# Optimization experiments

Hardware: AMD Instinct MI355X
Metric: run time of the kernel (lower is better)

The kernel has to match this reference:

```python
import jax, jax.numpy as jnp
import numpy as np
import math

DX = DZ = DATTN = DOUT = 1024
LX = LZ = 4096

def setup_inputs() -> dict:
    key = jax.random.key(0)
    ks = jax.random.split(key, 6)
    X = jax.random.normal(ks[0], (DX, LX), dtype=jnp.float32)
    Z = jax.random.normal(ks[1], (DZ, LZ), dtype=jnp.float32)
    mask = jax.random.randint(ks[2], (LZ, LX), 0, 2) > 0  # bool (lz, lx)
    Wq = jax.random.normal(ks[3], (DATTN, DX), dtype=jnp.float32) / math.sqrt(DATTN)
    bq = jnp.zeros((DATTN, 1), dtype=jnp.float32)
    Wk = jax.random.normal(ks[4], (DATTN, DZ), dtype=jnp.float32) / math.sqrt(DATTN)
    bk = jnp.zeros((DATTN, 1), dtype=jnp.float32)
    Wv = jax.random.normal(ks[5], (DOUT, DZ), dtype=jnp.float32) / math.sqrt(DOUT)
    bv = jnp.zeros((DOUT, 1), dtype=jnp.float32)
    return {"X": X, "Z": Z, "mask": mask, "Wq": Wq, "bq": bq,
            "Wk": Wk, "bk": bk, "Wv": Wv, "bv": bv}

def reference(X, Z, mask, Wq, bq, Wk, bk, Wv, bv):
    dattn_sqrt = math.sqrt(Wq.shape[0])
    q = Wq @ X + bq                      # (dattn, lx)
    k = Wk @ Z + bk                      # (dattn, lz)
    v = Wv @ Z + bv                      # (dout, lz)
    score = k.T @ q                      # (lz, lx)
    # masked_fill with -1000 happens BEFORE scaling, matching the original
    score = jnp.where(mask, score, jnp.float32(-1000.0))
    attn = jax.nn.softmax(score / dattn_sqrt, axis=0)  # softmax over lz (dim 0)
    return v @ attn                      # (dout, lx)
```

## Files before the change

kernel.cpp:

```cpp
#include <hip/hip_runtime.h>
#include <hip/hip_bf16.h>
#include <math.h>

constexpr int DXc = 1024;
constexpr int DZc = 1024;
constexpr int LXc = 4096;
constexpr int LZc = 4096;
constexpr int DAc = 1024;
constexpr int DOc = 1024;

typedef __attribute__((ext_vector_type(8))) short bf16x8;
typedef __attribute__((ext_vector_type(4))) float f32x4;

__device__ __forceinline__ ushort f2bf(float f) {
    __hip_bfloat16 h = __float2bfloat16(f);
    return *reinterpret_cast<ushort*>(&h);
}
__device__ __forceinline__ float bf2f(ushort u) {
    return __builtin_bit_cast(float, (unsigned)u << 16);
}

enum BiasMode { BIAS_NONE, BIAS_M, BIAS_N };

__device__ __forceinline__ void gemm_core(
    const ushort* __restrict__ A, const ushort* __restrict__ B,
    int K, int lda, int ldb, int m0, int n0, int kbase,
    ushort* As, ushort* Bs, f32x4 (*acc)[4])
{
    constexpr int BK = 32;
    const int tid = threadIdx.x;
    const int wv  = tid >> 6;
    const int wm  = (wv >> 1) * 64;
    const int wn  = (wv & 1) * 64;
    const int ln  = tid & 63;
    const int lrow = ln & 15;
    const int quad = ln >> 4;

    const int srow = tid >> 2;
    const int sseg = (tid & 3) * 8;
    const ushort* Ag = A + (size_t)(m0 + srow) * lda + sseg + kbase;
    const ushort* Bg = B + (size_t)(n0 + srow) * ldb + sseg + kbase;
    ushort* AsW = As + wv * 512;
    ushort* BsW = Bs + wv * 512;

    for (int k0 = 0; k0 < K; k0 += BK) {
        __syncthreads();
        __builtin_amdgcn_global_load_lds(
            (const __attribute__((address_space(1))) void*)(Ag + k0),
            (__attribute__((address_space(3))) void*)(AsW), 16, 0, 0);
        __builtin_amdgcn_global_load_lds(
            (const __attribute__((address_space(1))) void*)(Ag + (size_t)64 * lda + k0),
            (__attribute__((address_space(3))) void*)(AsW + 2048), 16, 0, 0);
        __builtin_amdgcn_global_load_lds(
            (const __attribute__((address_space(1))) void*)(Bg + k0),
            (__attribute__((address_space(3))) void*)(BsW), 16, 0, 0);
        __builtin_amdgcn_global_load_lds(
            (const __attribute__((address_space(1))) void*)(Bg + (size_t)64 * ldb + k0),
            (__attribute__((address_space(3))) void*)(BsW + 2048), 16, 0, 0);
        __syncthreads();

        bf16x8 af[4], bfr[4];
        #pragma unroll
        for (int t = 0; t < 4; ++t) {
            af[t]  = *reinterpret_cast<const bf16x8*>(&As[(wm + t * 16 + lrow) * BK + quad * 8]);
            bfr[t] = *reinterpret_cast<const bf16x8*>(&Bs[(wn + t * 16 + lrow) * BK + quad * 8]);
        }
        #pragma unroll
        for (int mi = 0; mi < 4; ++mi)
            #pragma unroll
            for (int nj = 0; nj < 4; ++nj)
                acc[mi][nj] = __builtin_amdgcn_mfma_f32_16x16x32_bf16(
                    af[mi], bfr[nj], acc[mi][nj], 0, 0, 0);
    }
}

template<BiasMode BMODE>
__device__ __forceinline__ void epi_bias_bf16(
    f32x4 (*acc)[4], const float* __restrict__ bias,
    ushort* __restrict__ C, int ldc, int m0, int n0)
{
    const int tid = threadIdx.x;
    const int wv  = tid >> 6;
    const int wm  = (wv >> 1) * 64;
    const int wn  = (wv & 1) * 64;
    const int lrow = tid & 15;
    const int quad = (tid & 63) >> 4;
    #pragma unroll
    for (int mi = 0; mi < 4; ++mi)
        #pragma unroll
        for (int r = 0; r < 4; ++r) {
            const int m = m0 + wm + mi * 16 + quad * 4 + r;
            const float bm = (BMODE == BIAS_M) ? bias[m] : 0.0f;
            #pragma unroll
            for (int nj = 0; nj < 4; ++nj) {
                const int n = n0 + wn + nj * 16 + lrow;
                const float v = acc[mi][nj][r] + ((BMODE == BIAS_N) ? bias[n] : bm);
                C[(size_t)m * ldc + n] = f2bf(v);
            }
        }
}

__global__ __launch_bounds__(256)
void proj_kernel(const ushort* __restrict__ XT, const ushort* __restrict__ ZT,
                 const ushort* __restrict__ Wqb, const ushort* __restrict__ Wkb,
                 const ushort* __restrict__ Wvb,
                 const float* __restrict__ bq, const float* __restrict__ bk,
                 const float* __restrict__ bv,
                 ushort* __restrict__ qT, ushort* __restrict__ kT,
                 ushort* __restrict__ vB)
{
    __shared__ __align__(16) ushort As[128 * 32];
    __shared__ __align__(16) ushort Bs[128 * 32];
    f32x4 acc[4][4] = {};
    int b = blockIdx.x;
    if (b < 256) {
        const int m0 = (b >> 3) * 128, n0 = (b & 7) * 128;
        gemm_core(XT, Wqb, DXc, DXc, DXc, m0, n0, 0, As, Bs, acc);
        epi_bias_bf16<BIAS_N>(acc, bq, qT, DAc, m0, n0);
    } else if (b < 512) {
        b -= 256;
        const int m0 = (b >> 3) * 128, n0 = (b & 7) * 128;
        gemm_core(ZT, Wkb, DZc, DZc, DZc, m0, n0, 0, As, Bs, acc);
        epi_bias_bf16<BIAS_N>(acc, bk, kT, DAc, m0, n0);
    } else {
        b -= 512;
        const int m0 = (b >> 5) * 128, n0 = (b & 31) * 128;
        gemm_core(Wvb, ZT, DZc, DZc, DZc, m0, n0, 0, As, Bs, acc);
        epi_bias_bf16<BIAS_M>(acc, bv, vB, LZc, m0, n0);
    }
}

__global__ __launch_bounds__(256)
void score_kernel(const ushort* __restrict__ qT, const ushort* __restrict__ kT,
                  ushort* __restrict__ sTb, const unsigned* __restrict__ bits,
                  float* __restrict__ rowsum)
{
    __shared__ __align__(16) ushort As[128 * 32];
    __shared__ __align__(16) ushort Bs[128 * 32];
    f32x4 acc[4][4] = {};
    const int b = blockIdx.x;
    const int m0 = (b >> 5) * 128, n0 = (b & 31) * 128;
    gemm_core(qT, kT, DAc, DAc, DAc, m0, n0, 0, As, Bs, acc);

    const int tid = threadIdx.x;
    const int wv  = tid >> 6;
    const int wm  = (wv >> 1) * 64;
    const int wn  = (wv & 1) * 64;
    const int lrow = tid & 15;
    const int quad = (tid & 63) >> 4;
    constexpr float scale = 1.0f / 32.0f;
    const int wbase = (n0 + wn) >> 5;

    #pragma unroll
    for (int mi = 0; mi < 4; ++mi) {
        #pragma unroll
        for (int r = 0; r < 4; ++r) {
            const int m = m0 + wm + mi * 16 + quad * 4 + r;
            const unsigned w0 = bits[(size_t)m * 128 + wbase];
            const unsigned w1 = bits[(size_t)m * 128 + wbase + 1];
            float rsum = 0.0f;
            #pragma unroll
            for (int nj = 0; nj < 4; ++nj) {
                const int nn = nj * 16 + lrow;
                const unsigned wsel = (nn < 32) ? w0 : w1;
                const bool mk = (wsel >> (nn & 31)) & 1u;
                float p = mk ? __expf(acc[mi][nj][r] * scale - 10.0f) : 0.0f;
                const ushort pb = f2bf(p);
                sTb[(size_t)m * LZc + (n0 + wn + nn)] = pb;
                rsum += bf2f(pb);
            }
            #pragma unroll
            for (int d = 1; d < 16; d <<= 1)
                rsum += __shfl_xor(rsum, d, 64);
            if (lrow == 0) atomicAdd(&rowsum[m], rsum);
        }
    }
}

__global__ __launch_bounds__(256)
void out_kernel(const ushort* __restrict__ vB, const ushort* __restrict__ sTb,
                float* __restrict__ P)
{
    __shared__ __align__(16) ushort As[128 * 32];
    __shared__ __align__(16) ushort Bs[128 * 32];
    f32x4 acc[4][4] = {};
    const int m0 = blockIdx.y * 128, n0 = blockIdx.x * 128;
    gemm_core(vB, sTb, LZc / 4, LZc, LZc, m0, n0, blockIdx.z * (LZc / 4), As, Bs, acc);

    float* Cf = P + (size_t)blockIdx.z * DOc * LXc;
    const int tid = threadIdx.x;
    const int wv  = tid >> 6;
    const int wm  = (wv >> 1) * 64;
    const int wn  = (wv & 1) * 64;
    const int lrow = tid & 15;
    const int quad = (tid & 63) >> 4;
    #pragma unroll
    for (int mi = 0; mi < 4; ++mi)
        #pragma unroll
        for (int r = 0; r < 4; ++r) {
            const int m = m0 + wm + mi * 16 + quad * 4 + r;
            #pragma unroll
            for (int nj = 0; nj < 4; ++nj)
                Cf[(size_t)m * LXc + (n0 + wn + nj * 16 + lrow)] = acc[mi][nj][r];
        }
}

__global__ __launch_bounds__(256)
void prep_kernel(const float* __restrict__ X, const float* __restrict__ Z,
                 const float* __restrict__ Wq, const float* __restrict__ Wk,
                 const float* __restrict__ Wv, const int* __restrict__ mask,
                 ushort* __restrict__ XT, ushort* __restrict__ ZT,
                 ushort* __restrict__ Wqb, ushort* __restrict__ Wkb,
                 ushort* __restrict__ Wvb, unsigned* __restrict__ bits)
{
    __shared__ float tile[32][33];
    const int tid = threadIdx.x;
    int b = blockIdx.x;

    if (b < 8192) {
        const float* in  = (b < 4096) ? X : Z;
        ushort*      out = (b < 4096) ? XT : ZT;
        const int local = b & 4095;
        const int c0 = (local & 127) * 32, r0 = (local >> 7) * 32;
        const int tx = tid & 31, ty = tid >> 5;
        #pragma unroll
        for (int i = 0; i < 32; i += 8)
            tile[ty + i][tx] = in[(size_t)(r0 + ty + i) * LXc + c0 + tx];
        __syncthreads();
        #pragma unroll
        for (int i = 0; i < 32; i += 8)
            out[(size_t)(c0 + ty + i) * DXc + r0 + tx] = f2bf(tile[tx][ty + i]);
        return;
    }
    if (b < 11264) {
        b -= 8192;
        const float* in  = (b < 1024) ? Wq : (b < 2048) ? Wk : Wv;
        ushort*      out = (b < 1024) ? Wqb : (b < 2048) ? Wkb : Wvb;
        const size_t i = ((size_t)(b & 1023) * 256 + tid) * 4;
        float4 f = *reinterpret_cast<const float4*>(in + i);
        ushort4 u;
        u.x = f2bf(f.x); u.y = f2bf(f.y); u.z = f2bf(f.z); u.w = f2bf(f.w);
        *reinterpret_cast<ushort4*>(out + i) = u;
        return;
    }
    b -= 11264;
    const int xb = b & 15, zb = b >> 4;
    const int x  = xb * 256 + tid;
    const int z0 = zb * 32;
    unsigned w = 0;
    #pragma unroll 8
    for (int i = 0; i < 32; ++i)
        w |= (mask[(size_t)(z0 + i) * LXc + x] != 0 ? 1u : 0u) << i;
    bits[(size_t)x * (LZc / 32) + zb] = w;
}

__global__ __launch_bounds__(256)
void reduce_kernel(const float* __restrict__ P, const float* __restrict__ rowsum,
                   float* __restrict__ out)
{
    constexpr size_t total = (size_t)DOc * LXc;
    const size_t i = ((size_t)blockIdx.x * 256 + threadIdx.x) * 4;
    float4 s = *reinterpret_cast<const float4*>(P + i);
    #pragma unroll
    for (int p = 1; p < 4; ++p) {
        const float4 t = *reinterpret_cast<const float4*>(P + (size_t)p * total + i);
        s.x += t.x; s.y += t.y; s.z += t.z; s.w += t.w;
    }
    const float4 l = *reinterpret_cast<const float4*>(rowsum + (i & (LXc - 1)));
    s.x /= fmaxf(l.x, 1e-30f);
    s.y /= fmaxf(l.y, 1e-30f);
    s.z /= fmaxf(l.z, 1e-30f);
    s.w /= fmaxf(l.w, 1e-30f);
    *reinterpret_cast<float4*>(out + i) = s;
}

extern "C" void kernel_launch(void* const* d_in, const int* in_sizes, int n_in,
                              void* d_out, int out_size, void* d_ws, size_t ws_size,
                              hipStream_t stream)
{
    const float* X    = (const float*)d_in[0];
    const float* Z    = (const float*)d_in[1];
    const int*   mask = (const int*)  d_in[2];
    const float* Wq   = (const float*)d_in[3];
    const float* bq   = (const float*)d_in[4];
    const float* Wk   = (const float*)d_in[5];
    const float* bk   = (const float*)d_in[6];
    const float* Wv   = (const float*)d_in[7];
    const float* bv   = (const float*)d_in[8];
    float* out = (float*)d_out;

    char* ws = (char*)d_ws;
    ushort*   XT     = (ushort*)(ws);
    ushort*   ZT     = (ushort*)(ws + ( 8ull << 20));
    ushort*   Wqb    = (ushort*)(ws + (16ull << 20));
    ushort*   Wkb    = (ushort*)(ws + (18ull << 20));
    ushort*   Wvb    = (ushort*)(ws + (20ull << 20));
    ushort*   qT     = (ushort*)(ws + (22ull << 20));
    ushort*   kT     = (ushort*)(ws + (30ull << 20));
    float*    P      = (float*) (ws);
    ushort*   vB     = (ushort*)(ws + (64ull << 20));
    ushort*   sTb    = (ushort*)(ws + (72ull << 20));
    unsigned* bits   = (unsigned*)(ws + (104ull << 20));
    float*    rowsum = (float*)  (ws + (106ull << 20));

    prep_kernel<<<dim3(13312), 256, 0, stream>>>(X, Z, Wq, Wk, Wv, mask,
                                                 XT, ZT, Wqb, Wkb, Wvb, bits);
    proj_kernel<<<dim3(768), 256, 0, stream>>>(XT, ZT, Wqb, Wkb, Wvb,
                                               bq, bk, bv, qT, kT, vB);
    hipMemsetAsync(rowsum, 0, LXc * sizeof(float), stream);
    score_kernel<<<dim3(1024), 256, 0, stream>>>(qT, kT, sTb, bits, rowsum);
    out_kernel<<<dim3(32, 8, 4), 256, 0, stream>>>(vB, sTb, P);
    reduce_kernel<<<dim3(DOc * LXc / 1024), 256, 0, stream>>>(P, rowsum, out);
}
```

Measured before the change: 325.2 us.

## Split masked exp into row kernel and fuse normalization into split-K atomic output

```diff
diff --git a/kernel.cpp b/kernel.cpp
--- a/kernel.cpp
+++ b/kernel.cpp
@@ -16,8 +16,11 @@
     __hip_bfloat16 h = __float2bfloat16(f);
     return *reinterpret_cast<ushort*>(&h);
 }
-__device__ __forceinline__ float bf2f(ushort u) {
-    return __builtin_bit_cast(float, (unsigned)u << 16);
+__device__ __forceinline__ float bflo(unsigned u) {
+    return __builtin_bit_cast(float, u << 16);
+}
+__device__ __forceinline__ float bfhi(unsigned u) {
+    return __builtin_bit_cast(float, u & 0xffff0000u);
 }
 
 enum BiasMode { BIAS_NONE, BIAS_M, BIAS_N };
@@ -132,8 +135,7 @@
 
 __global__ __launch_bounds__(256)
 void score_kernel(const ushort* __restrict__ qT, const ushort* __restrict__ kT,
-                  ushort* __restrict__ sTb, const unsigned* __restrict__ bits,
-                  float* __restrict__ rowsum)
+                  ushort* __restrict__ sTb)
 {
     __shared__ __align__(16) ushort As[128 * 32];
     __shared__ __align__(16) ushort Bs[128 * 32];
@@ -141,6 +143,55 @@
     const int b = blockIdx.x;
     const int m0 = (b >> 5) * 128, n0 = (b & 31) * 128;
     gemm_core(qT, kT, DAc, DAc, DAc, m0, n0, 0, As, Bs, acc);
+    epi_bias_bf16<BIAS_NONE>(acc, nullptr, sTb, LZc, m0, n0);
+}
+
+__global__ __launch_bounds__(256)
+void expsum_kernel(ushort* __restrict__ sTb, const unsigned* __restrict__ bits,
+                   float* __restrict__ rinv)
+{
+    const int x   = blockIdx.x;
+    const int tid = threadIdx.x;
+    ushort* row = sTb + (size_t)x * LZc;
+    constexpr float scale = 1.0f / 32.0f;
+
+    float sum = 0.0f;
+    #pragma unroll
+    for (int r = 0; r < 2; ++r) {
+        uint4 pk = *reinterpret_cast<uint4*>(row + (size_t)(r * 256 + tid) * 8);
+        unsigned* w = reinterpret_cast<unsigned*>(&pk);
+        const unsigned mb = (bits[(size_t)x * 128 + r * 64 + (tid >> 2)] >> ((tid & 3) * 8)) & 0xffu;
+        #pragma unroll
+        for (int j = 0; j < 4; ++j) {
+            const float lo = ((mb >> (2 * j))     & 1u) ? __expf(bflo(w[j]) * scale - 10.0f) : 0.0f;
+            const float hi = ((mb >> (2 * j + 1)) & 1u) ? __expf(bfhi(w[j]) * scale - 10.0f) : 0.0f;
+            const unsigned l = f2bf(lo), h = f2bf(hi);
+            w[j] = l | (h << 16);
+            sum += bflo(l) + bflo(h);
+        }
+        *reinterpret_cast<uint4*>(row + (size_t)(r * 256 + tid) * 8) = pk;
+    }
+    __shared__ float redsum[4];
+    #pragma unroll
+    for (int off = 32; off > 0; off >>= 1)
+        sum += __shfl_down(sum, off, 64);
+    if ((tid & 63) == 0) redsum[tid >> 6] = sum;
+    __syncthreads();
+    if (tid == 0) {
+        const float s = redsum[0] + redsum[1] + redsum[2] + redsum[3];
+        rinv[x] = 1.0f / fmaxf(s, 1e-35f);
+    }
+}
+
+__global__ __launch_bounds__(256)
+void out_kernel(const ushort* __restrict__ vB, const ushort* __restrict__ sTb,
+                const float* __restrict__ rinv, float* __restrict__ out)
+{
+    __shared__ __align__(16) ushort As[128 * 32];
+    __shared__ __align__(16) ushort Bs[128 * 32];
+    f32x4 acc[4][4] = {};
+    const int m0 = blockIdx.y * 128, n0 = blockIdx.x * 128;
+    gemm_core(vB, sTb, LZc / 4, LZc, LZc, m0, n0, blockIdx.z * (LZc / 4), As, Bs, acc);
 
     const int tid = threadIdx.x;
     const int wv  = tid >> 6;
@@ -148,52 +199,14 @@
     const int wn  = (wv & 1) * 64;
     const int lrow = tid & 15;
     const int quad = (tid & 63) >> 4;
-    constexpr float scale = 1.0f / 32.0f;
-    const int wbase = (n0 + wn) >> 5;
-
-    #pragma unroll
-    for (int mi = 0; mi < 4; ++mi) {
-        #pragma unroll
-        for (int r = 0; r < 4; ++r) {
-            const int m = m0 + wm + mi * 16 + quad * 4 + r;
-            const unsigned w0 = bits[(size_t)m * 128 + wbase];
-            const unsigned w1 = bits[(size_t)m * 128 + wbase + 1];
-            float rsum = 0.0f;
-            #pragma unroll
-            for (int nj = 0; nj < 4; ++nj) {
-                const int nn = nj * 16 + lrow;
-                const unsigned wsel = (nn < 32) ? w0 : w1;
-                const bool mk = (wsel >> (nn & 31)) & 1u;
-                float p = mk ? __expf(acc[mi][nj][r] * scale - 10.0f) : 0.0f;
-                const ushort pb = f2bf(p);
-                sTb[(size_t)m * LZc + (n0 + wn + nn)] = pb;
-                rsum += bf2f(pb);
-            }
-            #pragma unroll
-            for (int d = 1; d < 16; d <<= 1)
-                rsum += __shfl_xor(rsum, d, 64);
-            if (lrow == 0) atomicAdd(&rowsum[m], rsum);
-        }
-    }
-}
-
-__global__ __launch_bounds__(256)
-void out_kernel(const ushort* __restrict__ vB, const ushort* __restrict__ sTb,
-                float* __restrict__ P)
-{
-    __shared__ __align__(16) ushort As[128 * 32];
-    __shared__ __align__(16) ushort Bs[128 * 32];
-    f32x4 acc[4][4] = {};
-    const int m0 = blockIdx.y * 128, n0 = blockIdx.x * 128;
-    gemm_core(vB, sTb, LZc / 4, LZc, LZc, m0, n0, blockIdx.z * (LZc / 4), As, Bs, acc);
-
-    float* Cf = P + (size_t)blockIdx.z * DOc * LXc;
-    const int tid = threadIdx.x;
-    const int wv  = tid >> 6;
-    const int wm  = (wv >> 1) * 64;
-    const int wn  = (wv & 1) * 64;
-    const int lrow = tid & 15;
-    const int quad = (tid & 63) >> 4;
+
+    float inv[4];
+    int nn[4];
+    #pragma unroll
+    for (int nj = 0; nj < 4; ++nj) {
+        nn[nj]  = n0 + wn + nj * 16 + lrow;
+        inv[nj] = rinv[nn[nj]];
+    }
     #pragma unroll
     for (int mi = 0; mi < 4; ++mi)
         #pragma unroll
@@ -201,7 +214,7 @@
             const int m = m0 + wm + mi * 16 + quad * 4 + r;
             #pragma unroll
             for (int nj = 0; nj < 4; ++nj)
-                Cf[(size_t)m * LXc + (n0 + wn + nj * 16 + lrow)] = acc[mi][nj][r];
+                atomicAdd(&out[(size_t)m * LXc + nn[nj]], acc[mi][nj][r] * inv[nj]);
         }
 }
 
@@ -254,26 +267,6 @@
     bits[(size_t)x * (LZc / 32) + zb] = w;
 }
 
-__global__ __launch_bounds__(256)
-void reduce_kernel(const float* __restrict__ P, const float* __restrict__ rowsum,
-                   float* __restrict__ out)
-{
-    constexpr size_t total = (size_t)DOc * LXc;
-    const size_t i = ((size_t)blockIdx.x * 256 + threadIdx.x) * 4;
-    float4 s = *reinterpret_cast<const float4*>(P + i);
-    #pragma unroll
-    for (int p = 1; p < 4; ++p) {
-        const float4 t = *reinterpret_cast<const float4*>(P + (size_t)p * total + i);
-        s.x += t.x; s.y += t.y; s.z += t.z; s.w += t.w;
-    }
-    const float4 l = *reinterpret_cast<const float4*>(rowsum + (i & (LXc - 1)));
-    s.x /= fmaxf(l.x, 1e-30f);
-    s.y /= fmaxf(l.y, 1e-30f);
-    s.z /= fmaxf(l.z, 1e-30f);
-    s.w /= fmaxf(l.w, 1e-30f);
-    *reinterpret_cast<float4*>(out + i) = s;
-}
-
 extern "C" void kernel_launch(void* const* d_in, const int* in_sizes, int n_in,
                               void* d_out, int out_size, void* d_ws, size_t ws_size,
                               hipStream_t stream)
@@ -290,25 +283,24 @@
     float* out = (float*)d_out;
 
     char* ws = (char*)d_ws;
-    ushort*   XT     = (ushort*)(ws);
-    ushort*   ZT     = (ushort*)(ws + ( 8ull << 20));
-    ushort*   Wqb    = (ushort*)(ws + (16ull << 20));
-    ushort*   Wkb    = (ushort*)(ws + (18ull << 20));
-    ushort*   Wvb    = (ushort*)(ws + (20ull << 20));
-    ushort*   qT     = (ushort*)(ws + (22ull << 20));
-    ushort*   kT     = (ushort*)(ws + (30ull << 20));
-    float*    P      = (float*) (ws);
-    ushort*   vB     = (ushort*)(ws + (64ull << 20));
-    ushort*   sTb    = (ushort*)(ws + (72ull << 20));
-    unsigned* bits   = (unsigned*)(ws + (104ull << 20));
-    float*    rowsum = (float*)  (ws + (106ull << 20));
-
+    ushort*   XT   = (ushort*)(ws);
+    ushort*   ZT   = (ushort*)(ws + ( 8ull << 20));
+    ushort*   Wqb  = (ushort*)(ws + (16ull << 20));
+    ushort*   Wkb  = (ushort*)(ws + (18ull << 20));
+    ushort*   Wvb  = (ushort*)(ws + (20ull << 20));
+    ushort*   qT   = (ushort*)(ws + (22ull << 20));
+    ushort*   kT   = (ushort*)(ws + (30ull << 20));
+    ushort*   vB   = (ushort*)(ws + (38ull << 20));
+    ushort*   sTb  = (ushort*)(ws + (46ull << 20));
+    unsigned* bits = (unsigned*)(ws + (78ull << 20));
+    float*    rinv = (float*)  (ws + (80ull << 20));
+
+    hipMemsetAsync(out, 0, (size_t)DOc * LXc * sizeof(float), stream);
     prep_kernel<<<dim3(13312), 256, 0, stream>>>(X, Z, Wq, Wk, Wv, mask,
                                                  XT, ZT, Wqb, Wkb, Wvb, bits);
     proj_kernel<<<dim3(768), 256, 0, stream>>>(XT, ZT, Wqb, Wkb, Wvb,
                                                bq, bk, bv, qT, kT, vB);
-    hipMemsetAsync(rowsum, 0, LXc * sizeof(float), stream);
-    score_kernel<<<dim3(1024), 256, 0, stream>>>(qT, kT, sTb, bits, rowsum);
-    out_kernel<<<dim3(32, 8, 4), 256, 0, stream>>>(vB, sTb, P);
-    reduce_kernel<<<dim3(DOc * LXc / 1024), 256, 0, stream>>>(P, rowsum, out);
-}
+    score_kernel<<<dim3(1024), 256, 0, stream>>>(qT, kT, sTb);
+    expsum_kernel<<<dim3(LXc), 256, 0, stream>>>(sTb, bits, rinv);
+    out_kernel<<<dim3(32, 8, 4), 256, 0, stream>>>(vB, sTb, rinv, out);
+}
```

New measurement: 342.2 us. +5.2%, slower.
